# Kernel tuning notes

Measured on AMD Instinct MI355X. Metric: run time of the kernel, lower is better.

## Reference

```python
import jax, jax.numpy as jnp
import numpy as np

B, T, H, L, NH, FF, V, P = 8, 256, 768, 12, 12, 3072, 30522, 512
K, LH = 9, 256
DH = H // NH


def setup_inputs() -> dict:
    key = jax.random.key(0)
    kit = iter(jax.random.split(key, 48))
    rn = lambda shape: jax.random.normal(next(kit), shape, jnp.float32) * 0.02
    inp = {
        "input_ids": jax.random.randint(next(kit), (B, T), 0, V, dtype=jnp.int32),
        "attention_mask": jnp.ones((B, T), jnp.int32),
        "labels": jax.random.randint(next(kit), (B, T), 0, K, dtype=jnp.int32),
        "word_emb": rn((V, H)), "pos_emb": rn((P, H)), "type_emb": rn((2, H)),
        "emb_ln_g": jnp.ones((H,)), "emb_ln_b": jnp.zeros((H,)),
        "Wq": rn((L, H, H)), "bq": jnp.zeros((L, H)),
        "Wk": rn((L, H, H)), "bk": jnp.zeros((L, H)),
        "Wv": rn((L, H, H)), "bv": jnp.zeros((L, H)),
        "Wo": rn((L, H, H)), "bo": jnp.zeros((L, H)),
        "ln1_g": jnp.ones((L, H)), "ln1_b": jnp.zeros((L, H)),
        "Wf1": rn((L, H, FF)), "bf1": jnp.zeros((L, FF)),
        "Wf2": rn((L, FF, H)), "bf2": jnp.zeros((L, H)),
        "ln2_g": jnp.ones((L, H)), "ln2_b": jnp.zeros((L, H)),
        "w_ih_f": rn((4 * LH, H)), "w_hh_f": rn((4 * LH, LH)),
        "b_ih_f": jnp.zeros((4 * LH,)), "b_hh_f": jnp.zeros((4 * LH,)),
        "w_ih_b": rn((4 * LH, H)), "w_hh_b": rn((4 * LH, LH)),
        "b_ih_b": jnp.zeros((4 * LH,)), "b_hh_b": jnp.zeros((4 * LH,)),
        "W_clf": rn((2 * LH, K)), "b_clf": jnp.zeros((K,)),
        "crf_start": rn((K,)), "crf_end": rn((K,)), "crf_trans": rn((K, K)),
    }
    return inp


def _ln(x, g, b):
    m = jnp.mean(x, -1, keepdims=True)
    v = jnp.var(x, -1, keepdims=True)
    return (x - m) * jax.lax.rsqrt(v + 1e-12) * g + b


def _lstm(x, w_ih, w_hh, b_ih, b_hh, reverse):
    # PyTorch LSTM gate order: i, f, g, o. Precompute input gates: [T, B, 4*LH]
    xg = jnp.einsum('bth,gh->tbg', x, w_ih) + b_ih
    if reverse:
        xg = xg[::-1]

    def step(carry, g_in):
        h, c = carry
        g = g_in + h @ w_hh.T + b_hh
        i, f, gg, o = jnp.split(g, 4, axis=-1)
        c = jax.nn.sigmoid(f) * c + jax.nn.sigmoid(i) * jnp.tanh(gg)
        h = jax.nn.sigmoid(o) * jnp.tanh(c)
        return (h, c), h

    z = jnp.zeros((x.shape[0], w_hh.shape[1]), x.dtype)
    _, hs = jax.lax.scan(step, (z, z), xg)
    if reverse:
        hs = hs[::-1]
    return hs.transpose(1, 0, 2)  # [B, T, LH]


def reference(input_ids, attention_mask, labels, word_emb, pos_emb, type_emb,
              emb_ln_g, emb_ln_b, Wq, bq, Wk, bk, Wv, bv, Wo, bo, ln1_g, ln1_b,
              Wf1, bf1, Wf2, bf2, ln2_g, ln2_b, w_ih_f, w_hh_f, b_ih_f, b_hh_f,
              w_ih_b, w_hh_b, b_ih_b, b_hh_b, W_clf, b_clf,
              crf_start, crf_end, crf_trans):
    maskf = attention_mask.astype(jnp.float32)
    # ---- BERT embeddings ----
    x = word_emb[input_ids] + pos_emb[:T][None] + type_emb[0][None, None]
    x = _ln(x, emb_ln_g, emb_ln_b)
    attn_bias = (1.0 - maskf)[:, None, None, :] * -10000.0

    def layer(h, p):
        wq, bq_, wk, bk_, wv, bv_, wo, bo_, g1, b1, wf1, bf1_, wf2, bf2_, g2, b2 = p
        q = (h @ wq + bq_).reshape(B, T, NH, DH).transpose(0, 2, 1, 3)
        k = (h @ wk + bk_).reshape(B, T, NH, DH).transpose(0, 2, 1, 3)
        v = (h @ wv + bv_).reshape(B, T, NH, DH).transpose(0, 2, 1, 3)
        s = jnp.einsum('bhqd,bhkd->bhqk', q, k) * (1.0 / np.sqrt(DH)) + attn_bias
        ctx = jnp.einsum('bhqk,bhkd->bhqd', jax.nn.softmax(s, axis=-1), v)
        ctx = ctx.transpose(0, 2, 1, 3).reshape(B, T, H)
        a = _ln(h + ctx @ wo + bo_, g1, b1)
        f = jax.nn.gelu(a @ wf1 + bf1_, approximate=False) @ wf2 + bf2_
        return _ln(a + f, g2, b2), None

    x, _ = jax.lax.scan(layer, x, (Wq, bq, Wk, bk, Wv, bv, Wo, bo,
                                   ln1_g, ln1_b, Wf1, bf1, Wf2, bf2, ln2_g, ln2_b))

    # ---- BiLSTM + linear head -> emissions [B, T, K] ----
    hf = _lstm(x, w_ih_f, w_hh_f, b_ih_f, b_hh_f, False)
    hb = _lstm(x, w_ih_b, w_hh_b, b_ih_b, b_hh_b, True)
    em = jnp.concatenate([hf, hb], axis=-1) @ W_clf + b_clf

    # ---- CRF negative log-likelihood (torchcrf, reduction='mean'); model returns -llh ----
    # numerator: score of the gold path
    first = crf_start[labels[:, 0]] + jnp.take_along_axis(em[:, 0], labels[:, :1], 1)[:, 0]
    tr = crf_trans[labels[:, :-1], labels[:, 1:]]                      # [B, T-1]
    emt = jnp.take_along_axis(em[:, 1:], labels[:, 1:, None], 2)[..., 0]
    score = first + jnp.sum((tr + emt) * maskf[:, 1:], axis=1)
    ends = jnp.sum(maskf, axis=1).astype(jnp.int32) - 1
    last = jnp.take_along_axis(labels, ends[:, None], 1)[:, 0]
    score = score + crf_end[last]
    # denominator: log partition via forward algorithm
    alpha = crf_start[None] + em[:, 0]                                  # [B, K]

    def crf_step(alpha, inp):
        e_t, m_t = inp
        nxt = jax.nn.logsumexp(alpha[:, :, None] + crf_trans[None] + e_t[:, None, :], axis=1)
        return jnp.where(m_t[:, None] > 0, nxt, alpha), None

    alpha, _ = jax.lax.scan(crf_step, alpha,
                            (em[:, 1:].transpose(1, 0, 2), maskf[:, 1:].T))
    logZ = jax.nn.logsumexp(alpha + crf_end, axis=-1)
    return -jnp.mean(score - logZ)
```

## Files before the change

kernel.cpp:

```cpp
#include <hip/hip_runtime.h>
#include <math.h>

#define BB 8
#define TT 256
#define HH 768
#define NL 12
#define NH_ 12
#define DH_ 64
#define FF_ 3072
#define LH_ 256
#define KK_ 9

typedef unsigned char u8;
typedef unsigned short u16;
typedef unsigned int u32;
typedef __attribute__((ext_vector_type(4))) float f32x4;

static __device__ __forceinline__ float sigm_fast(float x) {
    return __builtin_amdgcn_rcpf(1.0f + __expf(-x));
}
static __device__ __forceinline__ float tanh_fast(float x) {
    return 1.0f - 2.0f * __builtin_amdgcn_rcpf(1.0f + __expf(2.0f * x));
}
static __device__ __forceinline__ float bf2f(u16 v) {
    return __uint_as_float(((u32)v) << 16);
}
template <bool HI>
static __device__ __forceinline__ u32 pk8(float a, float b, u32 old) {
    return (u32)__builtin_amdgcn_cvt_pk_fp8_f32(a, b, (int)old, HI);
}
static __device__ __forceinline__ u8 f8(float v) {
    return (u8)(pk8<false>(v, v, 0) & 0xff);
}

static __device__ __forceinline__ f32x4 mfma_fp8(long a, long b, f32x4 c) {
    return __builtin_amdgcn_mfma_f32_16x16x32_fp8_fp8(a, b, c, 0, 0, 0);
}

#define GLL16(gp, lp) __builtin_amdgcn_global_load_lds( \
    (const __attribute__((address_space(1))) void*)(gp), \
    (__attribute__((address_space(3))) void*)(lp), 16, 0, 0)

static __device__ __forceinline__ float block_sum(float v, float* red) {
    int tid = threadIdx.x;
#pragma unroll
    for (int o = 32; o > 0; o >>= 1) v += __shfl_xor(v, o);
    if ((tid & 63) == 0) red[tid >> 6] = v;
    __syncthreads();
    return red[0] + red[1] + red[2] + red[3];
}

__global__ __launch_bounds__(256) void embed_ln_kernel(
    const int* __restrict__ ids, const float* __restrict__ we, const float* __restrict__ pe,
    const float* __restrict__ te, const float* __restrict__ g, const float* __restrict__ b,
    float* __restrict__ out, u8* __restrict__ out8) {
    int row = blockIdx.x;
    int t = row % TT;
    int id = ids[row];
    __shared__ float xr[HH];
    __shared__ float reda[8], redb[8];
    int tid = threadIdx.x;
    float s = 0.f;
    for (int h = tid; h < HH; h += 256) {
        float v = we[(size_t)id * HH + h] + pe[(size_t)t * HH + h] + te[h];
        xr[h] = v; s += v;
    }
    float mean = block_sum(s, reda) * (1.0f / HH);
    float vs = 0.f;
    for (int h = tid; h < HH; h += 256) { float d = xr[h] - mean; vs += d * d; }
    float var = block_sum(vs, redb) * (1.0f / HH);
    float rstd = rsqrtf(var + 1e-12f);
    for (int h = tid; h < HH; h += 256) {
        float v = (xr[h] - mean) * rstd * g[h] + b[h];
        out[(size_t)row * HH + h] = v;
        out8[(size_t)row * HH + h] = f8(v);
    }
}

__global__ __launch_bounds__(256) void ln_residual_kernel(
    const float* __restrict__ a, const float* __restrict__ f,
    const float* __restrict__ g, const float* __restrict__ b,
    float* __restrict__ out, u8* __restrict__ out8) {
    int row = blockIdx.x;
    __shared__ float xr[HH];
    __shared__ float reda[8], redb[8];
    int tid = threadIdx.x;
    float s = 0.f;
    for (int h = tid; h < HH; h += 256) {
        float v = a[(size_t)row * HH + h] + f[(size_t)row * HH + h];
        xr[h] = v; s += v;
    }
    float mean = block_sum(s, reda) * (1.0f / HH);
    float vs = 0.f;
    for (int h = tid; h < HH; h += 256) { float d = xr[h] - mean; vs += d * d; }
    float var = block_sum(vs, redb) * (1.0f / HH);
    float rstd = rsqrtf(var + 1e-12f);
    for (int h = tid; h < HH; h += 256) {
        float v = (xr[h] - mean) * rstd * g[h] + b[h];
        out[(size_t)row * HH + h] = v;
        out8[(size_t)row * HH + h] = f8(v);
    }
}

template <bool LAYERS12>
__global__ __launch_bounds__(256) void conv_w_kernel(
    const float* __restrict__ Wq, const float* __restrict__ Wk,
    const float* __restrict__ Wv, const float* __restrict__ Wo,
    const float* __restrict__ Wf1, const float* __restrict__ Wf2,
    u8* __restrict__ wbuf) {
    __shared__ float tile[64][65];
    int bid = blockIdx.x;
    int layer = 0;
    if (LAYERS12) { layer = bid / 1728; bid -= layer * 1728; }
    size_t woff = (size_t)layer * 7077888;
    size_t hh2 = (size_t)layer * HH * HH;
    size_t hf2 = (size_t)layer * HH * FF_;
    const float* src; u8* dst; int R, C, bx, by;
    if (bid < 576) {
        int m = bid / 144, t = bid % 144;
        src = (m == 0 ? Wq + hh2 : m == 1 ? Wk + hh2 : m == 2 ? Wv + hh2 : Wo + hh2);
        dst = wbuf + woff + (size_t)m * 589824;
        R = 768; C = 768; bx = t % 12; by = t / 12;
    } else if (bid < 1152) {
        int t = bid - 576;
        src = Wf1 + hf2; dst = wbuf + woff + 2359296; R = 768; C = 3072;
        bx = t % 48; by = t / 48;
    } else {
        int t = bid - 1152;
        src = Wf2 + hf2; dst = wbuf + woff + 4718592; R = 3072; C = 768;
        bx = t % 12; by = t / 12;
    }
    int tx = threadIdx.x & 15, ty = threadIdx.x >> 4;
#pragma unroll
    for (int p = 0; p < 4; ++p) {
        int row = p * 16 + ty;
        float4 v = *(const float4*)&src[(size_t)(by * 64 + row) * C + bx * 64 + tx * 4];
        tile[row][tx * 4 + 0] = v.x; tile[row][tx * 4 + 1] = v.y;
        tile[row][tx * 4 + 2] = v.z; tile[row][tx * 4 + 3] = v.w;
    }
    __syncthreads();
    int rq = (threadIdx.x & 15) * 4, cc0 = threadIdx.x >> 4;
#pragma unroll
    for (int p = 0; p < 4; ++p) {
        int cc = p * 16 + cc0;
        u32 w0 = pk8<false>(tile[rq][cc], tile[rq + 1][cc], 0);
        w0 = pk8<true>(tile[rq + 2][cc], tile[rq + 3][cc], w0);
        *(u32*)&dst[(size_t)(bx * 64 + cc) * R + by * 64 + rq] = w0;
    }
}

__global__ __launch_bounds__(256) void prep_kernel(
    const float* __restrict__ whf, const float* __restrict__ whb,
    const float* __restrict__ wif, const float* __restrict__ wib,
    u8* __restrict__ wfrag8, u8* __restrict__ wihT) {
    int bid = blockIdx.x;
    int tid = threadIdx.x;
    if (bid < 256) {
        int idx = bid * 256 + tid;
        int dir = idx >> 15;
        int kt  = (idx >> 12) & 7;
        int mt  = (idx >> 6) & 63;
        int lane = idx & 63;
        const float* W = dir ? whb : whf;
        int row = mt * 16 + (lane & 15);
        int k = kt * 32 + (lane >> 4) * 8;
        const float* src = W + (size_t)row * LH_ + k;
        u32 w0 = pk8<false>(src[0], src[1], 0);
        w0 = pk8<true>(src[2], src[3], w0);
        u32 w1 = pk8<false>(src[4], src[5], 0);
        w1 = pk8<true>(src[6], src[7], w1);
        uint2 pk; pk.x = w0; pk.y = w1;
        size_t base = (size_t)(((dir * 8 + kt) * 64 + mt) * 64 + lane) * 8;
        *(uint2*)&wfrag8[base] = pk;
    } else {
        int which = (bid < 1024) ? 0 : 1;
        const float* src = which ? wib : wif;
        u8* dst = wihT + (size_t)which * 786432;
        int i = (bid - (which ? 1024 : 256)) * 256 + tid;
        float4 v = *(const float4*)&src[(size_t)i * 4];
        u32 w0 = pk8<false>(v.x, v.y, 0);
        w0 = pk8<true>(v.z, v.w, w0);
        *(u32*)&dst[(size_t)i * 4] = w0;
    }
}

template <int BROWS>
__device__ __forceinline__ void stage8(
    const u8* __restrict__ S, int r0, int K, int k0, u8 (*lds)[128], int w, int lane) {
    int rsub = lane >> 3;
    int ap = lane & 7;
    constexpr int INSTS = BROWS / 32;
#pragma unroll
    for (int i = 0; i < INSTS; ++i) {
        int row0 = (w * INSTS + i) * 8;
        int row = row0 + rsub;
        int al = ap ^ (row & 7);
        GLL16(S + (size_t)(r0 + row) * K + k0 + al * 16, &lds[row0][0]);
    }
}

static __device__ __forceinline__ long lds8_read(const u8 (*lds)[128], int row, int g) {
    int a = g >> 1;
    int phys = a ^ (row & 7);
    return *(const long*)&lds[row][phys * 16 + (g & 1) * 8];
}

template <int BM, int BN, bool GELU, bool OUTF8, bool QKVW>
__global__ __launch_bounds__(256) void gemm3_kernel(
    const u8* __restrict__ A, const u8* __restrict__ BT,
    const float* __restrict__ b0, const float* __restrict__ b1, const float* __restrict__ b2,
    int seg, float* __restrict__ C, u8* __restrict__ C8, u8* __restrict__ vT,
    int M, int N, int K) {
    __shared__ u8 Als[2][BM][128];
    __shared__ u8 Bls[2][BN][128];
    int tid = threadIdx.x, lane = tid & 63, w = tid >> 6;
    int m0 = blockIdx.y * BM, n0 = blockIdx.x * BN;
    int wr = w >> 1, wc = w & 1;
    int l15 = lane & 15, q = lane >> 4;
    constexpr int MI = BM / 32;
    constexpr int NJ = BN / 32;

    f32x4 acc[MI][NJ];
#pragma unroll
    for (int mi = 0; mi < MI; ++mi)
#pragma unroll
        for (int nj = 0; nj < NJ; ++nj) acc[mi][nj] = (f32x4){0.f, 0.f, 0.f, 0.f};

    stage8<BM>(A, m0, K, 0, Als[0], w, lane);
    stage8<BN>(BT, n0, K, 0, Bls[0], w, lane);
    __syncthreads();
    int KT = K >> 7, cur = 0;
    for (int kt = 0; kt < KT; ++kt) {
        if (kt + 1 < KT) {
            stage8<BM>(A, m0, K, (kt + 1) << 7, Als[cur ^ 1], w, lane);
            stage8<BN>(BT, n0, K, (kt + 1) << 7, Bls[cur ^ 1], w, lane);
        }
#pragma unroll
        for (int ks = 0; ks < 4; ++ks) {
            int g = ks * 4 + q;
            long bfr[NJ];
#pragma unroll
            for (int nj = 0; nj < NJ; ++nj)
                bfr[nj] = lds8_read(Bls[cur], wc * (BN / 2) + nj * 16 + l15, g);
#pragma unroll
            for (int mi = 0; mi < MI; ++mi) {
                long a = lds8_read(Als[cur], wr * (BM / 2) + mi * 16 + l15, g);
#pragma unroll
                for (int nj = 0; nj < NJ; ++nj)
                    acc[mi][nj] = mfma_fp8(a, bfr[nj], acc[mi][nj]);
            }
        }
        __syncthreads();
        cur ^= 1;
    }

    int rbase = m0 + wr * (BM / 2) + q * 4;
    int cbase = n0 + wc * (BN / 2) + l15;
#pragma unroll
    for (int mi = 0; mi < MI; ++mi) {
#pragma unroll
        for (int nj = 0; nj < NJ; ++nj) {
            int col = cbase + nj * 16;
            int cc = col;
            const float* bp;
            if (cc < seg) bp = b0;
            else if (cc < 2 * seg) { bp = b1; cc -= seg; }
            else { bp = b2; cc -= 2 * seg; }
            float bias = bp[cc];
            if (QKVW && col >= 1536) {
                int hh = (col - 1536) >> 6, dl = (col - 1536) & 63;
                int brow = rbase + mi * 16;
                int bb = brow >> 8, t0 = brow & 255;
                u32 pkv = pk8<false>(acc[mi][nj][0] + bias, acc[mi][nj][1] + bias, 0);
                pkv = pk8<true>(acc[mi][nj][2] + bias, acc[mi][nj][3] + bias, pkv);
                *(u32*)&vT[(size_t)((bb * NH_ + hh) * DH_ + dl) * TT + t0] = pkv;
            } else {
#pragma unroll
                for (int j = 0; j < 4; ++j) {
                    int row = rbase + mi * 16 + j;
                    float v = acc[mi][nj][j] + bias;
                    if (GELU) v = 0.5f * v * (1.0f + erff(v * 0.70710678118654752f));
                    if (OUTF8 || QKVW) C8[(size_t)row * N + col] = f8(v);
                    else               C[(size_t)row * N + col] = v;
                }
            }
        }
    }
}

__global__ __launch_bounds__(256) void attn_mfma_kernel(
    const u8* __restrict__ qkv8, const u8* __restrict__ vT,
    const int* __restrict__ mask, u8* __restrict__ ctx8) {
    int bid = blockIdx.x;
    int qb = bid & 3;
    int bh = bid >> 2;
    int b = bh / NH_, h = bh % NH_;
    int tid = threadIdx.x, lane = tid & 63, w = tid >> 6;
    int l15 = lane & 15, g4 = lane >> 4;
    __shared__ float bias_s[TT];
    __shared__ u8 P[64][260];
    for (int i = tid; i < TT; i += 256)
        bias_s[i] = (1.0f - (float)mask[b * TT + i]) * -10000.0f;
    __syncthreads();

    size_t qoff = (size_t)(b * TT + qb * 64 + w * 16 + l15) * 2304 + h * DH_ + g4 * 8;
    long aq0 = *(const long*)&qkv8[qoff];
    long aq1 = *(const long*)&qkv8[qoff + 32];

    f32x4 sacc[16];
#pragma unroll
    for (int nt = 0; nt < 16; ++nt) sacc[nt] = (f32x4){0.f, 0.f, 0.f, 0.f};
#pragma unroll
    for (int nt = 0; nt < 16; ++nt) {
        size_t koff = (size_t)(b * TT + nt * 16 + l15) * 2304 + 768 + h * DH_ + g4 * 8;
        long b0 = *(const long*)&qkv8[koff];
        long b1 = *(const long*)&qkv8[koff + 32];
        sacc[nt] = mfma_fp8(aq0, b0, sacc[nt]);
        sacc[nt] = mfma_fp8(aq1, b1, sacc[nt]);
    }
    float m[4] = {-1e30f, -1e30f, -1e30f, -1e30f};
#pragma unroll
    for (int nt = 0; nt < 16; ++nt) {
        float bv = bias_s[nt * 16 + l15];
#pragma unroll
        for (int j = 0; j < 4; ++j) {
            float s = sacc[nt][j] * 0.125f + bv;
            sacc[nt][j] = s;
            m[j] = fmaxf(m[j], s);
        }
    }
#pragma unroll
    for (int j = 0; j < 4; ++j) {
        m[j] = fmaxf(m[j], __shfl_xor(m[j], 1));
        m[j] = fmaxf(m[j], __shfl_xor(m[j], 2));
        m[j] = fmaxf(m[j], __shfl_xor(m[j], 4));
        m[j] = fmaxf(m[j], __shfl_xor(m[j], 8));
    }
    float l[4] = {0.f, 0.f, 0.f, 0.f};
#pragma unroll
    for (int nt = 0; nt < 16; ++nt) {
#pragma unroll
        for (int j = 0; j < 4; ++j) {
            float p = __expf(sacc[nt][j] - m[j]);
            sacc[nt][j] = p;
            l[j] += p;
        }
    }
#pragma unroll
    for (int j = 0; j < 4; ++j) {
        l[j] += __shfl_xor(l[j], 1);
        l[j] += __shfl_xor(l[j], 2);
        l[j] += __shfl_xor(l[j], 4);
        l[j] += __shfl_xor(l[j], 8);
    }
#pragma unroll
    for (int nt = 0; nt < 16; ++nt) {
#pragma unroll
        for (int j = 0; j < 4; ++j)
            P[w * 16 + g4 * 4 + j][nt * 16 + l15] = f8(sacc[nt][j]);
    }
    f32x4 oacc[4];
#pragma unroll
    for (int nt4 = 0; nt4 < 4; ++nt4) oacc[nt4] = (f32x4){0.f, 0.f, 0.f, 0.f};
    const u8* vbase = vT + (size_t)(bh * DH_) * TT;
#pragma unroll
    for (int ks = 0; ks < 8; ++ks) {
        long pa = *(const long*)&P[w * 16 + l15][ks * 32 + g4 * 8];
#pragma unroll
        for (int nt4 = 0; nt4 < 4; ++nt4) {
            long bv = *(const long*)&vbase[(size_t)(nt4 * 16 + l15) * TT + ks * 32 + g4 * 8];
            oacc[nt4] = mfma_fp8(pa, bv, oacc[nt4]);
        }
    }
    float inv[4];
#pragma unroll
    for (int j = 0; j < 4; ++j) inv[j] = __builtin_amdgcn_rcpf(l[j]);
    int rowg = b * TT + qb * 64 + w * 16 + g4 * 4;
#pragma unroll
    for (int nt4 = 0; nt4 < 4; ++nt4) {
        int col = h * DH_ + nt4 * 16 + l15;
#pragma unroll
        for (int j = 0; j < 4; ++j)
            ctx8[(size_t)(rowg + j) * HH + col] = f8(oacc[nt4][j] * inv[j]);
    }
}

__global__ __launch_bounds__(1024, 4) void lstm13_kernel(
    const float* __restrict__ xg, const u8* __restrict__ wfrag8,
    const float* __restrict__ bhh_f, const float* __restrict__ bhh_b,
    float* __restrict__ hf, float* __restrict__ hb) {
    int dir = blockIdx.x;
    const u8* wf8 = wfrag8 + (size_t)dir * 262144;
    const float* bhh = dir ? bhh_b : bhh_f;
    float* hout = dir ? hb : hf;
    int tid = threadIdx.x, lane = tid & 63, wid = tid >> 6;
    __shared__ u8 wlds[4 * 64 * 512];
    __shared__ u8 h_f8[16][280];
    __shared__ u16 g_bf[1024][10];
    for (int i = tid; i < 16 * 280; i += 1024) ((u8*)h_f8)[i] = 0;
#pragma unroll
    for (int c = 0; c < 8; ++c) {
        int off = wid * 8192 + c * 1024;
        GLL16(wf8 + off + lane * 16, &wlds[off]);
    }
    long wst[4][4];
#pragma unroll
    for (int kt = 0; kt < 4; ++kt)
#pragma unroll
        for (int m = 0; m < 4; ++m) {
            wst[kt][m] = *(const long*)&wf8[(size_t)(((4 + kt) * 64) + wid * 4 + m) * 512 + lane * 8];
            asm volatile("" : "+v"(wst[kt][m]));
        }
    int l15 = lane & 15, qq = lane >> 4;
    int j = tid & 255;
    int bq = (tid >> 8) * 2;
    float bi_ = bhh[j], bf_ = bhh[256 + j], bg_ = bhh[512 + j], bo_ = bhh[768 + j];
    float c_s[2] = {0.f, 0.f};
    __syncthreads();
    for (int step = 0; step < TT; ++step) {
        int t = dir ? (TT - 1 - step) : step;
        float xgi[2], xgf[2], xgg[2], xgo[2];
#pragma unroll
        for (int bi = 0; bi < 2; ++bi) {
            size_t xa = ((size_t)((bq + bi) * TT + t)) * 2048 + (size_t)dir * 1024;
            xgi[bi] = xg[xa + j];
            xgf[bi] = xg[xa + 256 + j];
            xgg[bi] = xg[xa + 512 + j];
            xgo[bi] = xg[xa + 768 + j];
        }
        f32x4 acc[4];
#pragma unroll
        for (int m = 0; m < 4; ++m) acc[m] = (f32x4){0.f, 0.f, 0.f, 0.f};
#pragma unroll
        for (int kt = 0; kt < 4; ++kt) {
            long hfr = *(const long*)&h_f8[l15][kt * 32 + qq * 8];
#pragma unroll
            for (int m = 0; m < 4; ++m) {
                long a = *(const long*)&wlds[(size_t)(kt * 64 + wid * 4 + m) * 512 + lane * 8];
                acc[m] = mfma_fp8(a, hfr, acc[m]);
            }
        }
#pragma unroll
        for (int kt = 0; kt < 4; ++kt) {
            long hfr = *(const long*)&h_f8[l15][(4 + kt) * 32 + qq * 8];
#pragma unroll
            for (int m = 0; m < 4; ++m)
                acc[m] = mfma_fp8(wst[kt][m], hfr, acc[m]);
        }
        if (l15 < 8) {
#pragma unroll
            for (int m = 0; m < 4; ++m) {
                int R = (wid * 4 + m) * 16 + qq * 4;
#pragma unroll
                for (int jj = 0; jj < 4; ++jj)
                    g_bf[R + jj][l15] = (u16)(__float_as_uint(acc[m][jj]) >> 16);
            }
        }
        __syncthreads();
#pragma unroll
        for (int bi = 0; bi < 2; ++bi) {
            int b = bq + bi;
            float gi = xgi[bi] + bi_ + bf2f(g_bf[j][b]);
            float gf = xgf[bi] + bf_ + bf2f(g_bf[256 + j][b]);
            float gg = xgg[bi] + bg_ + bf2f(g_bf[512 + j][b]);
            float go = xgo[bi] + bo_ + bf2f(g_bf[768 + j][b]);
            float cc = sigm_fast(gf) * c_s[bi] + sigm_fast(gi) * tanh_fast(gg);
            c_s[bi] = cc;
            float hh = sigm_fast(go) * tanh_fast(cc);
            h_f8[b][j] = f8(hh);
            hout[((size_t)(b * TT + t)) * LH_ + j] = hh;
        }
        __syncthreads();
    }
}

__global__ __launch_bounds__(256) void clf_kernel(
    const float* __restrict__ hf, const float* __restrict__ hb,
    const float* __restrict__ W, const float* __restrict__ bias, float* __restrict__ em) {
    int idx = blockIdx.x * blockDim.x + threadIdx.x;
    if (idx >= BB * TT * KK_) return;
    int row = idx / KK_, j = idx % KK_;
    float acc = bias[j];
    const float* hfp = hf + (size_t)row * LH_;
    const float* hbp = hb + (size_t)row * LH_;
    for (int kk = 0; kk < LH_; ++kk) acc += hfp[kk] * W[kk * KK_ + j];
    for (int kk = 0; kk < LH_; ++kk) acc += hbp[kk] * W[(LH_ + kk) * KK_ + j];
    em[idx] = acc;
}

__global__ __launch_bounds__(512) void crf2_kernel(
    const float* __restrict__ em, const int* __restrict__ labels, const int* __restrict__ mask,
    const float* __restrict__ cstart, const float* __restrict__ cend,
    const float* __restrict__ ctrans, float* __restrict__ out) {
    __shared__ float trans_s[81];
    __shared__ float res[8];
    int tid = threadIdx.x;
    int b = tid >> 6;
    int l = tid & 63;
    if (tid < 81) trans_s[tid] = ctrans[tid];
    __syncthreads();
    int lc = (l < 9) ? l : 0;
    float tcol[9];
#pragma unroll
    for (int i = 0; i < 9; ++i) tcol[i] = trans_s[i * 9 + lc];
    float alpha = (l < 9) ? cstart[lc] + em[(size_t)b * TT * KK_ + lc] : -1e30f;
    for (int t = 1; t < TT; ++t) {
        float e_t = (l < 9) ? em[((size_t)b * TT + t) * KK_ + lc] : 0.f;
        float m = -1e30f;
        float av[9];
#pragma unroll
        for (int i = 0; i < 9; ++i) {
            av[i] = __shfl(alpha, i) + tcol[i];
            m = fmaxf(m, av[i]);
        }
        float s = 0.f;
#pragma unroll
        for (int i = 0; i < 9; ++i) s += expf(av[i] - m);
        float nv = m + logf(s) + e_t;
        bool upd = (mask[b * TT + t] > 0) && (l < 9);
        alpha = upd ? nv : alpha;
    }
    float z = (l < 9) ? alpha + cend[lc] : -1e30f;
    float zm = z;
#pragma unroll
    for (int o = 32; o > 0; o >>= 1) zm = fmaxf(zm, __shfl_xor(zm, o));
    float zs = (l < 9) ? expf(z - zm) : 0.f;
#pragma unroll
    for (int o = 32; o > 0; o >>= 1) zs += __shfl_xor(zs, o);
    float logZ = zm + logf(zs);
    float sc = 0.f;
    int cnt = 0;
    for (int t = l; t < TT; t += 64) {
        cnt += mask[b * TT + t];
        if (t == 0) {
            int l0 = labels[b * TT];
            sc += cstart[l0] + em[(size_t)b * TT * KK_ + l0];
        } else {
            int lp = labels[b * TT + t - 1];
            int lt = labels[b * TT + t];
            sc += (trans_s[lp * KK_ + lt] + em[((size_t)b * TT + t) * KK_ + lt]) *
                  (float)mask[b * TT + t];
        }
    }
#pragma unroll
    for (int o = 32; o > 0; o >>= 1) { sc += __shfl_xor(sc, o); cnt += __shfl_xor(cnt, o); }
    if (l == 0) {
        int last = labels[b * TT + (cnt - 1)];
        sc += cend[last];
        res[b] = sc - logZ;
    }
    __syncthreads();
    if (tid == 0) {
        float acc = 0.f;
        for (int bb = 0; bb < BB; ++bb) acc += res[bb];
        out[0] = -acc / (float)BB;
    }
}

extern "C" void kernel_launch(void* const* d_in, const int* in_sizes, int n_in,
                              void* d_out, int out_size, void* d_ws, size_t ws_size,
                              hipStream_t stream) {
    const int* input_ids = (const int*)d_in[0];
    const int* attn_mask = (const int*)d_in[1];
    const int* labels    = (const int*)d_in[2];
    const float* word_emb = (const float*)d_in[3];
    const float* pos_emb  = (const float*)d_in[4];
    const float* type_emb = (const float*)d_in[5];
    const float* emb_ln_g = (const float*)d_in[6];
    const float* emb_ln_b = (const float*)d_in[7];
    const float* Wq = (const float*)d_in[8];
    const float* bq = (const float*)d_in[9];
    const float* Wk = (const float*)d_in[10];
    const float* bk = (const float*)d_in[11];
    const float* Wv = (const float*)d_in[12];
    const float* bv = (const float*)d_in[13];
    const float* Wo = (const float*)d_in[14];
    const float* bo = (const float*)d_in[15];
    const float* ln1_g = (const float*)d_in[16];
    const float* ln1_b = (const float*)d_in[17];
    const float* Wf1 = (const float*)d_in[18];
    const float* bf1 = (const float*)d_in[19];
    const float* Wf2 = (const float*)d_in[20];
    const float* bf2 = (const float*)d_in[21];
    const float* ln2_g = (const float*)d_in[22];
    const float* ln2_b = (const float*)d_in[23];
    const float* w_ih_f = (const float*)d_in[24];
    const float* w_hh_f = (const float*)d_in[25];
    const float* b_ih_f = (const float*)d_in[26];
    const float* b_hh_f = (const float*)d_in[27];
    const float* w_ih_b = (const float*)d_in[28];
    const float* w_hh_b = (const float*)d_in[29];
    const float* b_ih_b = (const float*)d_in[30];
    const float* b_hh_b = (const float*)d_in[31];
    const float* W_clf  = (const float*)d_in[32];
    const float* b_clf  = (const float*)d_in[33];
    const float* crf_start = (const float*)d_in[34];
    const float* crf_end   = (const float*)d_in[35];
    const float* crf_trans = (const float*)d_in[36];

    const size_t NTOK = (size_t)BB * TT;
    const size_t SZ = NTOK * HH;

    float* ws = (float*)d_ws;
    float* x    = ws;
    float* scr  = x + SZ;
    float* tmp  = scr + NTOK * 2304;
    float* ab   = tmp + SZ;
    float* xg   = ab + SZ;
    u8* x_f8    = (u8*)(xg + NTOK * 2048);
    u8* ab_f8   = x_f8 + SZ;
    u8* ctx_f8  = ab_f8 + SZ;
    u8* big_f8  = ctx_f8 + SZ;
    u8* qkv8    = big_f8 + NTOK * (size_t)FF_;
    u8* vT      = qkv8 + NTOK * 2304;
    u8* wihT    = vT + SZ;
    u8* wfrag8  = wihT + 1572864;
    u8* wbuf    = wfrag8 + 524288;
    const size_t base_off = (size_t)((u8*)wbuf - (u8*)d_ws);
    bool big = ws_size >= base_off + 12ull * 7077888ull + (1u << 20);

    float* hf = scr;
    float* hb = scr + 524288;
    float* em = scr + 1048576;

    embed_ln_kernel<<<NTOK, 256, 0, stream>>>(input_ids, word_emb, pos_emb, type_emb,
                                              emb_ln_g, emb_ln_b, x, x_f8);
    prep_kernel<<<1792, 256, 0, stream>>>(w_hh_f, w_hh_b, w_ih_f, w_ih_b, wfrag8, wihT);
    if (big)
        conv_w_kernel<true><<<1728 * 12, 256, 0, stream>>>(Wq, Wk, Wv, Wo, Wf1, Wf2, wbuf);

    dim3 gQKV(2304 / 128, NTOK / 128);
    dim3 gH(HH / 64, NTOK / 64);
    dim3 gF1(FF_ / 128, NTOK / 128);
    dim3 gG(2048 / 128, NTOK / 128);

    for (int l = 0; l < NL; ++l) {
        u8* wb = big ? wbuf + (size_t)l * 7077888 : wbuf;
        if (!big)
            conv_w_kernel<false><<<1728, 256, 0, stream>>>(
                Wq + (size_t)l * HH * HH, Wk + (size_t)l * HH * HH,
                Wv + (size_t)l * HH * HH, Wo + (size_t)l * HH * HH,
                Wf1 + (size_t)l * HH * FF_, Wf2 + (size_t)l * FF_ * HH, wb);

        const float* bq_l = bq + (size_t)l * HH;
        const float* bk_l = bk + (size_t)l * HH;
        const float* bv_l = bv + (size_t)l * HH;
        const float* bo_l = bo + (size_t)l * HH;
        const float* g1 = ln1_g + (size_t)l * HH;
        const float* b1 = ln1_b + (size_t)l * HH;
        const float* bf1_l = bf1 + (size_t)l * FF_;
        const float* bf2_l = bf2 + (size_t)l * HH;
        const float* g2 = ln2_g + (size_t)l * HH;
        const float* b2 = ln2_b + (size_t)l * HH;

        gemm3_kernel<128, 128, false, false, true><<<gQKV, 256, 0, stream>>>(
            x_f8, wb, bq_l, bk_l, bv_l, 768, nullptr, qkv8, vT, NTOK, 2304, HH);
        attn_mfma_kernel<<<BB * NH_ * 4, 256, 0, stream>>>(qkv8, vT, attn_mask, ctx_f8);
        gemm3_kernel<64, 64, false, false, false><<<gH, 256, 0, stream>>>(
            ctx_f8, wb + 1769472, bo_l, bo_l, bo_l, 768, tmp, nullptr, nullptr, NTOK, HH, HH);
        ln_residual_kernel<<<NTOK, 256, 0, stream>>>(x, tmp, g1, b1, ab, ab_f8);
        gemm3_kernel<128, 128, true, true, false><<<gF1, 256, 0, stream>>>(
            ab_f8, wb + 2359296, bf1_l, bf1_l, bf1_l, FF_, nullptr, big_f8, nullptr, NTOK, FF_, HH);
        gemm3_kernel<64, 64, false, false, false><<<gH, 256, 0, stream>>>(
            big_f8, wb + 4718592, bf2_l, bf2_l, bf2_l, 768, tmp, nullptr, nullptr, NTOK, HH, FF_);
        ln_residual_kernel<<<NTOK, 256, 0, stream>>>(ab, tmp, g2, b2, x, x_f8);
    }

    gemm3_kernel<128, 128, false, false, false><<<gG, 256, 0, stream>>>(
        x_f8, wihT, b_ih_f, b_ih_b, b_ih_b, 1024, xg, nullptr, nullptr, NTOK, 2048, HH);

    lstm13_kernel<<<2, 1024, 0, stream>>>(xg, wfrag8, b_hh_f, b_hh_b, hf, hb);
    clf_kernel<<<(BB * TT * KK_ + 255) / 256, 256, 0, stream>>>(hf, hb, W_clf, b_clf, em);
    crf2_kernel<<<1, 512, 0, stream>>>(em, labels, attn_mask, crf_start, crf_end, crf_trans,
                                       (float*)d_out);
}
```

Baseline: 2.114 ms.

## Split LSTM across batch blocks and store input gates as bf16

After: 1.978 ms. 1.07x faster.

```diff
diff --git a/kernel.cpp b/kernel.cpp
--- a/kernel.cpp
+++ b/kernel.cpp
@@ -24,6 +24,11 @@
 }
 static __device__ __forceinline__ float bf2f(u16 v) {
     return __uint_as_float(((u32)v) << 16);
+}
+static __device__ __forceinline__ u16 f2b16(float f) {
+    u32 u = __float_as_uint(f);
+    u += 0x7fffu + ((u >> 16) & 1u);
+    return (u16)(u >> 16);
 }
 template <bool HI>
 static __device__ __forceinline__ u32 pk8(float a, float b, u32 old) {
@@ -205,12 +210,12 @@
     return *(const long*)&lds[row][phys * 16 + (g & 1) * 8];
 }
 
-template <int BM, int BN, bool GELU, bool OUTF8, bool QKVW>
+template <int BM, int BN, int OM, bool GELU, bool QKVW>
 __global__ __launch_bounds__(256) void gemm3_kernel(
     const u8* __restrict__ A, const u8* __restrict__ BT,
     const float* __restrict__ b0, const float* __restrict__ b1, const float* __restrict__ b2,
-    int seg, float* __restrict__ C, u8* __restrict__ C8, u8* __restrict__ vT,
-    int M, int N, int K) {
+    int seg, float* __restrict__ C, u8* __restrict__ C8, u16* __restrict__ C16,
+    u8* __restrict__ vT, int M, int N, int K) {
     __shared__ u8 Als[2][BM][128];
     __shared__ u8 Bls[2][BN][128];
     int tid = threadIdx.x, lane = tid & 63, w = tid >> 6;
@@ -280,8 +285,9 @@
                     int row = rbase + mi * 16 + j;
                     float v = acc[mi][nj][j] + bias;
                     if (GELU) v = 0.5f * v * (1.0f + erff(v * 0.70710678118654752f));
-                    if (OUTF8 || QKVW) C8[(size_t)row * N + col] = f8(v);
-                    else               C[(size_t)row * N + col] = v;
+                    if (OM == 1) C8[(size_t)row * N + col] = f8(v);
+                    else if (OM == 2) C16[(size_t)row * N + col] = f2b16(v);
+                    else C[(size_t)row * N + col] = v;
                 }
             }
         }
@@ -385,11 +391,12 @@
     }
 }
 
-__global__ __launch_bounds__(1024, 4) void lstm13_kernel(
-    const float* __restrict__ xg, const u8* __restrict__ wfrag8,
+__global__ __launch_bounds__(1024, 4) void lstm14_kernel(
+    const u16* __restrict__ xgb, const u8* __restrict__ wfrag8,
     const float* __restrict__ bhh_f, const float* __restrict__ bhh_b,
     float* __restrict__ hf, float* __restrict__ hb) {
-    int dir = blockIdx.x;
+    int dir = blockIdx.x >> 3;
+    int bat = blockIdx.x & 7;
     const u8* wf8 = wfrag8 + (size_t)dir * 262144;
     const float* bhh = dir ? bhh_b : bhh_f;
     float* hout = dir ? hb : hf;
@@ -413,20 +420,18 @@
         }
     int l15 = lane & 15, qq = lane >> 4;
     int j = tid & 255;
-    int bq = (tid >> 8) * 2;
     float bi_ = bhh[j], bf_ = bhh[256 + j], bg_ = bhh[512 + j], bo_ = bhh[768 + j];
-    float c_s[2] = {0.f, 0.f};
+    float c_r = 0.f;
     __syncthreads();
     for (int step = 0; step < TT; ++step) {
         int t = dir ? (TT - 1 - step) : step;
-        float xgi[2], xgf[2], xgg[2], xgo[2];
-#pragma unroll
-        for (int bi = 0; bi < 2; ++bi) {
-            size_t xa = ((size_t)((bq + bi) * TT + t)) * 2048 + (size_t)dir * 1024;
-            xgi[bi] = xg[xa + j];
-            xgf[bi] = xg[xa + 256 + j];
-            xgg[bi] = xg[xa + 512 + j];
-            xgo[bi] = xg[xa + 768 + j];
+        float xgi = 0.f, xgf = 0.f, xgg = 0.f, xgo = 0.f;
+        if (tid < 256) {
+            size_t xa = ((size_t)(bat * TT + t)) * 2048 + (size_t)dir * 1024;
+            xgi = bf2f(xgb[xa + j]);
+            xgf = bf2f(xgb[xa + 256 + j]);
+            xgg = bf2f(xgb[xa + 512 + j]);
+            xgo = bf2f(xgb[xa + 768 + j]);
         }
         f32x4 acc[4];
 #pragma unroll
@@ -447,28 +452,26 @@
             for (int m = 0; m < 4; ++m)
                 acc[m] = mfma_fp8(wst[kt][m], hfr, acc[m]);
         }
-        if (l15 < 8) {
+        if (l15 == 0) {
 #pragma unroll
             for (int m = 0; m < 4; ++m) {
                 int R = (wid * 4 + m) * 16 + qq * 4;
 #pragma unroll
                 for (int jj = 0; jj < 4; ++jj)
-                    g_bf[R + jj][l15] = (u16)(__float_as_uint(acc[m][jj]) >> 16);
+                    g_bf[R + jj][0] = (u16)(__float_as_uint(acc[m][jj]) >> 16);
             }
         }
         __syncthreads();
-#pragma unroll
-        for (int bi = 0; bi < 2; ++bi) {
-            int b = bq + bi;
-            float gi = xgi[bi] + bi_ + bf2f(g_bf[j][b]);
-            float gf = xgf[bi] + bf_ + bf2f(g_bf[256 + j][b]);
-            float gg = xgg[bi] + bg_ + bf2f(g_bf[512 + j][b]);
-            float go = xgo[bi] + bo_ + bf2f(g_bf[768 + j][b]);
-            float cc = sigm_fast(gf) * c_s[bi] + sigm_fast(gi) * tanh_fast(gg);
-            c_s[bi] = cc;
+        if (tid < 256) {
+            float gi = xgi + bi_ + bf2f(g_bf[j][0]);
+            float gf = xgf + bf_ + bf2f(g_bf[256 + j][0]);
+            float gg = xgg + bg_ + bf2f(g_bf[512 + j][0]);
+            float go = xgo + bo_ + bf2f(g_bf[768 + j][0]);
+            float cc = sigm_fast(gf) * c_r + sigm_fast(gi) * tanh_fast(gg);
+            c_r = cc;
             float hh = sigm_fast(go) * tanh_fast(cc);
-            h_f8[b][j] = f8(hh);
-            hout[((size_t)(b * TT + t)) * LH_ + j] = hh;
+            h_f8[0][j] = f8(hh);
+            hout[((size_t)(bat * TT + t)) * LH_ + j] = hh;
         }
         __syncthreads();
     }
@@ -606,8 +609,8 @@
     float* scr  = x + SZ;
     float* tmp  = scr + NTOK * 2304;
     float* ab   = tmp + SZ;
-    float* xg   = ab + SZ;
-    u8* x_f8    = (u8*)(xg + NTOK * 2048);
+    u16* xg16   = (u16*)(ab + SZ);
+    u8* x_f8    = (u8*)(xg16 + NTOK * 2048);
     u8* ab_f8   = x_f8 + SZ;
     u8* ctx_f8  = ab_f8 + SZ;
     u8* big_f8  = ctx_f8 + SZ;
@@ -653,23 +656,27 @@
         const float* g2 = ln2_g + (size_t)l * HH;
         const float* b2 = ln2_b + (size_t)l * HH;
 
-        gemm3_kernel<128, 128, false, false, true><<<gQKV, 256, 0, stream>>>(
-            x_f8, wb, bq_l, bk_l, bv_l, 768, nullptr, qkv8, vT, NTOK, 2304, HH);
+        gemm3_kernel<128, 128, 1, false, true><<<gQKV, 256, 0, stream>>>(
+            x_f8, wb, bq_l, bk_l, bv_l, 768, nullptr, qkv8, nullptr, vT, NTOK, 2304, HH);
         attn_mfma_kernel<<<BB * NH_ * 4, 256, 0, stream>>>(qkv8, vT, attn_mask, ctx_f8);
-        gemm3_kernel<64, 64, false, false, false><<<gH, 256, 0, stream>>>(
-            ctx_f8, wb + 1769472, bo_l, bo_l, bo_l, 768, tmp, nullptr, nullptr, NTOK, HH, HH);
+        gemm3_kernel<64, 64, 0, false, false><<<gH, 256, 0, stream>>>(
+            ctx_f8, wb + 1769472, bo_l, bo_l, bo_l, 768, tmp, nullptr, nullptr, nullptr,
+            NTOK, HH, HH);
         ln_residual_kernel<<<NTOK, 256, 0, stream>>>(x, tmp, g1, b1, ab, ab_f8);
-        gemm3_kernel<128, 128, true, true, false><<<gF1, 256, 0, stream>>>(
-            ab_f8, wb + 2359296, bf1_l, bf1_l, bf1_l, FF_, nullptr, big_f8, nullptr, NTOK, FF_, HH);
-        gemm3_kernel<64, 64, false, false, false><<<gH, 256, 0, stream>>>(
-            big_f8, wb + 4718592, bf2_l, bf2_l, bf2_l, 768, tmp, nullptr, nullptr, NTOK, HH, FF_);
+        gemm3_kernel<128, 128, 1, true, false><<<gF1, 256, 0, stream>>>(
+            ab_f8, wb + 2359296, bf1_l, bf1_l, bf1_l, FF_, nullptr, big_f8, nullptr, nullptr,
+            NTOK, FF_, HH);
+        gemm3_kernel<64, 64, 0, false, false><<<gH, 256, 0, stream>>>(
+            big_f8, wb + 4718592, bf2_l, bf2_l, bf2_l, 768, tmp, nullptr, nullptr, nullptr,
+            NTOK, HH, FF_);
         ln_residual_kernel<<<NTOK, 256, 0, stream>>>(ab, tmp, g2, b2, x, x_f8);
     }
 
-    gemm3_kernel<128, 128, false, false, false><<<gG, 256, 0, stream>>>(
-        x_f8, wihT, b_ih_f, b_ih_b, b_ih_b, 1024, xg, nullptr, nullptr, NTOK, 2048, HH);
-
-    lstm13_kernel<<<2, 1024, 0, stream>>>(xg, wfrag8, b_hh_f, b_hh_b, hf, hb);
+    gemm3_kernel<128, 128, 2, false, false><<<gG, 256, 0, stream>>>(
+        x_f8, wihT, b_ih_f, b_ih_b, b_ih_b, 1024, nullptr, nullptr, xg16, nullptr,
+        NTOK, 2048, HH);
+
+    lstm14_kernel<<<16, 1024, 0, stream>>>(xg16, wfrag8, b_hh_f, b_hh_b, hf, hb);
     clf_kernel<<<(BB * TT * KK_ + 255) / 256, 256, 0, stream>>>(hf, hb, W_clf, b_clf, em);
     crf2_kernel<<<1, 512, 0, stream>>>(em, labels, attn_mask, crf_start, crf_end, crf_trans,
                                        (float*)d_out);
```
